# Performance work log

Hardware: AMD Instinct MI355X
Metric: run time of the kernel (lower is better)

The kernel has to match this reference:

```python
import jax, jax.numpy as jnp
import numpy as np

HIDDEN = 4096
N_HEADS = 32
N_KV_HEADS = 8
HEAD_DIM = 128
ROPE_THETA = 1e6
EPS = 1e-6
T = 2048


def setup_inputs() -> dict:
    key = jax.random.key(0)
    k1, k2, k3, k4, k5 = jax.random.split(key, 5)
    q_size = N_HEADS * HEAD_DIM
    kv_size = N_KV_HEADS * HEAD_DIM
    return {
        "positions": jnp.arange(T, dtype=jnp.int32),
        "hidden_states": jax.random.normal(k1, (T, HIDDEN), dtype=jnp.float32),
        "Wqkv": jax.random.normal(k2, (HIDDEN, q_size + 2 * kv_size), dtype=jnp.float32) * (HIDDEN ** -0.5),
        "Wo": jax.random.normal(k3, (q_size, HIDDEN), dtype=jnp.float32) * (q_size ** -0.5),
        "q_norm_w": jnp.ones((HEAD_DIM,), dtype=jnp.float32) + 0.01 * jax.random.normal(k4, (HEAD_DIM,), dtype=jnp.float32),
        "k_norm_w": jnp.ones((HEAD_DIM,), dtype=jnp.float32) + 0.01 * jax.random.normal(k5, (HEAD_DIM,), dtype=jnp.float32),
    }


def _rmsnorm(x, w):
    var = jnp.mean(jnp.square(x), axis=-1, keepdims=True)
    return x * jax.lax.rsqrt(var + EPS) * w


def _rope(x, positions):
    # NeoX-style rotate-half RoPE, rotary_dim == head_dim. x: [T, H, D]
    half = HEAD_DIM // 2
    inv_freq = 1.0 / (ROPE_THETA ** (jnp.arange(0, half, dtype=jnp.float32) / half))
    ang = positions.astype(jnp.float32)[:, None] * inv_freq  # [T, D/2]
    cos = jnp.cos(ang)[:, None, :]  # [T, 1, D/2]
    sin = jnp.sin(ang)[:, None, :]
    x1, x2 = x[..., :half], x[..., half:]
    return jnp.concatenate([x1 * cos - x2 * sin, x2 * cos + x1 * sin], axis=-1)


def reference(positions, hidden_states, Wqkv, Wo, q_norm_w, k_norm_w):
    q_size = N_HEADS * HEAD_DIM
    kv_size = N_KV_HEADS * HEAD_DIM
    qkv = hidden_states @ Wqkv  # [T, q+2kv]
    q = qkv[:, :q_size].reshape(-1, N_HEADS, HEAD_DIM)
    k = qkv[:, q_size:q_size + kv_size].reshape(-1, N_KV_HEADS, HEAD_DIM)
    v = qkv[:, q_size + kv_size:].reshape(-1, N_KV_HEADS, HEAD_DIM)
    q = _rmsnorm(q, q_norm_w)
    k = _rmsnorm(k, k_norm_w)
    q = _rope(q, positions)
    k = _rope(k, positions)
    rep = N_HEADS // N_KV_HEADS
    k = jnp.repeat(k, rep, axis=1)  # [T, 32, D]
    v = jnp.repeat(v, rep, axis=1)
    scale = HEAD_DIM ** -0.5
    scores = jnp.einsum('thd,shd->hts', q, k) * scale  # [H, T, T]
    t = hidden_states.shape[0]
    causal = jnp.tril(jnp.ones((t, t), dtype=bool))
    scores = jnp.where(causal[None, :, :], scores, jnp.finfo(scores.dtype).min)
    probs = jax.nn.softmax(scores, axis=-1)
    o = jnp.einsum('hts,shd->thd', probs, v)  # [T, H, D]
    return o.reshape(t, -1) @ Wo  # [T, hidden]
```

## Files before the change

kernel.cpp:

```cpp
#include <hip/hip_runtime.h>

#define T_SEQ 2048
#define HID   4096
#define NH    32
#define NKV   8
#define HD    128
#define QS    (NH*HD)
#define KVS   (NKV*HD)
#define QKVN  (QS + 2*KVS)

typedef unsigned short u16;
typedef __attribute__((ext_vector_type(8))) __bf16 bf16x8;
typedef __attribute__((ext_vector_type(8))) unsigned short u16x8;
typedef __attribute__((ext_vector_type(4))) unsigned short u16x4;
typedef __attribute__((ext_vector_type(4))) float f32x4;

__device__ __forceinline__ u16 f2bu(float x) {
  unsigned u = __builtin_bit_cast(unsigned, x);
  return (u16)((u + 0x7fffu + ((u >> 16) & 1u)) >> 16);
}
__device__ __forceinline__ float bu2f(u16 v) {
  unsigned u = ((unsigned)v) << 16;
  return __builtin_bit_cast(float, u);
}
__device__ __forceinline__ void gload16(const void* g, void* l) {
  __builtin_amdgcn_global_load_lds((const __attribute__((address_space(1))) void*)g,
                                   (__attribute__((address_space(3))) void*)l, 16, 0, 0);
}

__global__ void k_cvt(const float* __restrict__ in, u16* __restrict__ out, int n8) {
  for (int i = blockIdx.x * blockDim.x + threadIdx.x; i < n8; i += gridDim.x * blockDim.x) {
    const float4* p = (const float4*)in + (size_t)i * 2;
    float4 a = p[0], b = p[1];
    u16x8 v;
    v[0]=f2bu(a.x); v[1]=f2bu(a.y); v[2]=f2bu(a.z); v[3]=f2bu(a.w);
    v[4]=f2bu(b.x); v[5]=f2bu(b.y); v[6]=f2bu(b.z); v[7]=f2bu(b.w);
    *((u16x8*)out + i) = v;
  }
}

__global__ void k_transcvt(const float* __restrict__ in, u16* __restrict__ out, int R, int C) {
  __shared__ float tile[32][33];
  int c0 = blockIdx.x * 32, r0 = blockIdx.y * 32;
  int tx = threadIdx.x & 31, ty = threadIdx.x >> 5;
#pragma unroll
  for (int g = 0; g < 4; ++g)
    tile[ty + g * 8][tx] = in[(size_t)(r0 + ty + g * 8) * C + c0 + tx];
  __syncthreads();
#pragma unroll
  for (int g = 0; g < 4; ++g) {
    int cc = g * 8 + ty;
    out[(size_t)(c0 + cc) * R + r0 + tx] = f2bu(tile[tx][cc]);
  }
}

template<int OUTF32>
__global__ __launch_bounds__(256, 2)
void k_gemm(const u16* __restrict__ A, const u16* __restrict__ Bt,
            void* __restrict__ C, int K, int ldc) {
  __shared__ u16 sA[128 * 64];
  __shared__ u16 sB[128 * 64];
  const int tid = threadIdx.x;
  const int w = tid >> 6, lane = tid & 63, lo = lane & 15, hi = lane >> 4;
  const int wr = w >> 1, wc = w & 1;
  const int bm = blockIdx.y * 128, bn = blockIdx.x * 128;
  f32x4 acc[4][4] = {};
  const int nk = K >> 6;
  for (int kt = 0; kt < nk; ++kt) {
    const int kbase = kt * 64;
#pragma unroll
    for (int i = 0; i < 4; ++i) {
      int c = i * 256 + tid;
      int row = c >> 3, o8 = (c & 7) * 8;
      gload16(A + (size_t)(bm + row) * K + kbase + o8, sA + c * 8);
      gload16(Bt + (size_t)(bn + row) * K + kbase + o8, sB + c * 8);
    }
    __syncthreads();
#pragma unroll
    for (int kc = 0; kc < 2; ++kc) {
      bf16x8 af[4], bfr[4];
#pragma unroll
      for (int m = 0; m < 4; ++m)
        af[m] = *(const bf16x8*)(sA + (wr * 64 + m * 16 + lo) * 64 + kc * 32 + hi * 8);
#pragma unroll
      for (int n = 0; n < 4; ++n)
        bfr[n] = *(const bf16x8*)(sB + (wc * 64 + n * 16 + lo) * 64 + kc * 32 + hi * 8);
#pragma unroll
      for (int m = 0; m < 4; ++m)
#pragma unroll
        for (int n = 0; n < 4; ++n)
          acc[m][n] = __builtin_amdgcn_mfma_f32_16x16x32_bf16(af[m], bfr[n], acc[m][n], 0, 0, 0);
    }
    __syncthreads();
  }
#pragma unroll
  for (int m = 0; m < 4; ++m)
#pragma unroll
    for (int n = 0; n < 4; ++n) {
      int col = bn + wc * 64 + n * 16 + lo;
#pragma unroll
      for (int r = 0; r < 4; ++r) {
        int row = bm + wr * 64 + m * 16 + hi * 4 + r;
        float v = acc[m][n][r];
        if (OUTF32) ((float*)C)[(size_t)row * ldc + col] = v;
        else        ((u16*)C)[(size_t)row * ldc + col] = f2bu(v);
      }
    }
}

__global__ void k_normrope(const u16* __restrict__ qkv, const int* __restrict__ pos,
                           const float* __restrict__ qw, const float* __restrict__ kw,
                           u16* __restrict__ qb, u16* __restrict__ kb, u16* __restrict__ vb) {
  const int t = blockIdx.x;
  const int tid = threadIdx.x, w = tid >> 6, lane = tid & 63;
  const float p = (float)pos[t];
  const int d0 = lane * 2;
  const int j = d0 & 63;
  const float L2T_64 = 19.931568569324174f / 64.0f;
  float ang0 = p * exp2f(-(float)j * L2T_64);
  float ang1 = p * exp2f(-(float)(j + 1) * L2T_64);
  float c0 = cosf(ang0), s0 = sinf(ang0);
  float c1 = cosf(ang1), s1 = sinf(ang1);
  const bool hiHalf = lane >= 32;
  for (int it = 0; it < 10; ++it) {
    int h = it * 4 + w;
    bool isq = h < NH;
    int base = t * QKVN + (isq ? h * HD : QS + (h - NH) * HD);
    float x0 = bu2f(qkv[base + d0]);
    float x1 = bu2f(qkv[base + d0 + 1]);
    float ss = x0 * x0 + x1 * x1;
#pragma unroll
    for (int off = 1; off < 64; off <<= 1) ss += __shfl_xor(ss, off);
    float inv = rsqrtf(ss * (1.0f / 128.0f) + 1e-6f);
    const float* nw = isq ? qw : kw;
    float y0 = x0 * inv * nw[d0];
    float y1 = x1 * inv * nw[d0 + 1];
    float z0 = __shfl_xor(y0, 32);
    float z1 = __shfl_xor(y1, 32);
    float r0 = hiHalf ? (y0 * c0 + z0 * s0) : (y0 * c0 - z0 * s0);
    float r1 = hiHalf ? (y1 * c1 + z1 * s1) : (y1 * c1 - z1 * s1);
    u16* dst = isq ? (qb + ((size_t)h * T_SEQ + t) * HD)
                   : (kb + ((size_t)(h - NH) * T_SEQ + t) * HD);
    dst[d0] = f2bu(r0);
    dst[d0 + 1] = f2bu(r1);
  }
  for (int i = tid; i < KVS; i += 256) {
    int kvh = i >> 7, d = i & 127;
    vb[((size_t)kvh * T_SEQ + t) * HD + d] = qkv[t * QKVN + QS + KVS + i];
  }
}

__global__ __launch_bounds__(256, 4)
void k_attn(const u16* __restrict__ qb, const u16* __restrict__ kb,
            const u16* __restrict__ vb, u16* __restrict__ ao) {
  __shared__ u16 Ks[64 * 128];
  __shared__ u16 Vt[128 * 64];
  __shared__ u16 Ps[4][16 * 64];
  const int h = blockIdx.y, kvh = h >> 2;
  const int q0 = blockIdx.x * 64;
  const int tid = threadIdx.x, w = tid >> 6, lane = tid & 63, lo = lane & 15, hi = lane >> 4;
  const int lo7 = lane & 7;
  const int qr0 = q0 + w * 16;
  bf16x8 qf[4];
  const u16* Qp = qb + ((size_t)h * T_SEQ + qr0 + lo) * HD;
#pragma unroll
  for (int kc = 0; kc < 4; ++kc) qf[kc] = *(const bf16x8*)(Qp + kc * 32 + hi * 8);
  f32x4 o[8] = {};
  float mrow[4], ssum[4];
#pragma unroll
  for (int r = 0; r < 4; ++r) { mrow[r] = -1e30f; ssum[r] = 0.f; }
  const float scale = 0.08838834764831845f;
  const int nkt = blockIdx.x + 1;
  const u16* Kb = kb + (size_t)kvh * T_SEQ * HD;
  const u16* Vb = vb + (size_t)kvh * T_SEQ * HD;
  const int krow = tid >> 4;
  const int kg = (tid & 15) ^ (krow & 7);
  const int vkvc = tid & 15, vfc = tid >> 4;

  for (int kt = 0; kt < nkt; ++kt) {
#pragma unroll
    for (int i = 0; i < 4; ++i)
      gload16(Kb + (size_t)(kt * 64 + i * 16 + krow) * HD + kg * 8,
              Ks + i * 2048 + tid * 8);
    {
      u16x8 vv0 = *(const u16x8*)(Vb + (size_t)(kt * 64 + vkvc * 4 + 0) * HD + vfc * 8);
      u16x8 vv1 = *(const u16x8*)(Vb + (size_t)(kt * 64 + vkvc * 4 + 1) * HD + vfc * 8);
      u16x8 vv2 = *(const u16x8*)(Vb + (size_t)(kt * 64 + vkvc * 4 + 2) * HD + vfc * 8);
      u16x8 vv3 = *(const u16x8*)(Vb + (size_t)(kt * 64 + vkvc * 4 + 3) * HD + vfc * 8);
#pragma unroll
      for (int e = 0; e < 8; ++e) {
        int feat = vfc * 8 + e;
        int gp = (vkvc >> 1) ^ (feat & 7);
        u16x4 pk; pk[0] = vv0[e]; pk[1] = vv1[e]; pk[2] = vv2[e]; pk[3] = vv3[e];
        *(u16x4*)(Vt + feat * 64 + gp * 8 + (vkvc & 1) * 4) = pk;
      }
    }
    __syncthreads();
    f32x4 sa[4] = {};
#pragma unroll
    for (int kc = 0; kc < 4; ++kc) {
#pragma unroll
      for (int n = 0; n < 4; ++n) {
        int row = n * 16 + lo;
        bf16x8 kf = *(const bf16x8*)(Ks + row * 128 + (((kc * 4 + hi) ^ lo7) * 8));
        sa[n] = __builtin_amdgcn_mfma_f32_16x16x32_bf16(qf[kc], kf, sa[n], 0, 0, 0);
      }
    }
    float pvv[4][4], pmax[4];
#pragma unroll
    for (int r = 0; r < 4; ++r) {
      int qi = qr0 + hi * 4 + r;
      float pm = -1e30f;
#pragma unroll
      for (int n = 0; n < 4; ++n) {
        int kj = kt * 64 + n * 16 + lo;
        float sv = (kj <= qi) ? sa[n][r] * scale : -1e30f;
        pvv[n][r] = sv;
        pm = fmaxf(pm, sv);
      }
#pragma unroll
      for (int off = 1; off < 16; off <<= 1) pm = fmaxf(pm, __shfl_xor(pm, off));
      pmax[r] = pm;
    }
#pragma unroll
    for (int r = 0; r < 4; ++r) {
      float mnew = fmaxf(mrow[r], pmax[r]);
      float corr = __expf(mrow[r] - mnew);
      mrow[r] = mnew;
      float ps = 0.f;
#pragma unroll
      for (int n = 0; n < 4; ++n) {
        float p = __expf(pvv[n][r] - mnew);
        pvv[n][r] = p; ps += p;
      }
#pragma unroll
      for (int off = 1; off < 16; off <<= 1) ps += __shfl_xor(ps, off);
      ssum[r] = ssum[r] * corr + ps;
#pragma unroll
      for (int nf = 0; nf < 8; ++nf) o[nf][r] *= corr;
    }
    u16* Pw = Ps[w];
#pragma unroll
    for (int n = 0; n < 4; ++n) {
      int gcol = n * 2 + (lo >> 3);
#pragma unroll
      for (int r = 0; r < 4; ++r) {
        int row = hi * 4 + r;
        Pw[row * 64 + ((gcol ^ (row & 7)) * 8) + lo7] = f2bu(pvv[n][r]);
      }
    }
#pragma unroll
    for (int ks = 0; ks < 2; ++ks) {
      bf16x8 pf = *(const bf16x8*)(Pw + lo * 64 + (((ks * 4 + hi) ^ lo7) * 8));
#pragma unroll
      for (int nf = 0; nf < 8; ++nf) {
        int feat = nf * 16 + lo;
        bf16x8 vf = *(const bf16x8*)(Vt + feat * 64 + (((ks * 4 + hi) ^ lo7) * 8));
        o[nf] = __builtin_amdgcn_mfma_f32_16x16x32_bf16(pf, vf, o[nf], 0, 0, 0);
      }
    }
    __syncthreads();
  }
#pragma unroll
  for (int r = 0; r < 4; ++r) ssum[r] = 1.0f / ssum[r];
#pragma unroll
  for (int nf = 0; nf < 8; ++nf)
#pragma unroll
    for (int r = 0; r < 4; ++r) {
      int row = qr0 + hi * 4 + r;
      ao[(size_t)row * HID + h * HD + nf * 16 + lo] = f2bu(o[nf][r] * ssum[r]);
    }
}

extern "C" void kernel_launch(void* const* d_in, const int* in_sizes, int n_in,
                              void* d_out, int out_size, void* d_ws, size_t ws_size,
                              hipStream_t stream) {
  (void)in_sizes; (void)n_in; (void)out_size; (void)ws_size;
  const int*   positions = (const int*)d_in[0];
  const float* hs   = (const float*)d_in[1];
  const float* wqkv = (const float*)d_in[2];
  const float* wo   = (const float*)d_in[3];
  const float* qnw  = (const float*)d_in[4];
  const float* knw  = (const float*)d_in[5];
  char* ws = (char*)d_ws;

  u16* hsb   = (u16*)d_out;
  u16* qbuf  = (u16*)d_out + 8388608;
  u16* wqkvT = (u16*)(ws + 0);
  u16* woT   = (u16*)(ws + 50331648);
  u16* qkvb  = (u16*)(ws + 83886080);
  u16* kbuf  = (u16*)(ws + 109051904);
  u16* vbuf  = (u16*)(ws + 113246208);
  u16* aob   = (u16*)(ws + 0);

  k_cvt<<<2048, 256, 0, stream>>>(hs, hsb, (T_SEQ * HID) / 8);
  k_transcvt<<<dim3(QKVN / 32, HID / 32), 256, 0, stream>>>(wqkv, wqkvT, HID, QKVN);
  k_transcvt<<<dim3(HID / 32, QS / 32), 256, 0, stream>>>(wo, woT, QS, HID);
  k_gemm<0><<<dim3(QKVN / 128, T_SEQ / 128), 256, 0, stream>>>(hsb, wqkvT, qkvb, HID, QKVN);
  k_normrope<<<T_SEQ, 256, 0, stream>>>(qkvb, positions, qnw, knw, qbuf, kbuf, vbuf);
  k_attn<<<dim3(T_SEQ / 64, NH), 256, 0, stream>>>(qbuf, kbuf, vbuf, aob);
  k_gemm<1><<<dim3(HID / 128, T_SEQ / 128), 256, 0, stream>>>(aob, woT, d_out, QS, HID);
}
```

Before: 648.6 us.

## Pair causal attention query tiles per block and vectorize weight transpose-convert

Each attention block now handles two query tiles, x and 31-x, so every block does the same amount of causal work and the grid shrinks from 32x32 to 16x32 blocks. This removes the tail imbalance of the triangular causal workload. The weight transpose/convert kernel moves to 64x64 tiles with float4 loads and 16-byte bf16 stores to cut memory transactions. The risk is fewer blocks in flight for attention (512 on a large GPU) and more serial work per block.

```diff
diff --git a/kernel.cpp b/kernel.cpp
--- a/kernel.cpp
+++ b/kernel.cpp
@@ -40,18 +40,28 @@
 }
 
 __global__ void k_transcvt(const float* __restrict__ in, u16* __restrict__ out, int R, int C) {
-  __shared__ float tile[32][33];
-  int c0 = blockIdx.x * 32, r0 = blockIdx.y * 32;
-  int tx = threadIdx.x & 31, ty = threadIdx.x >> 5;
-#pragma unroll
-  for (int g = 0; g < 4; ++g)
-    tile[ty + g * 8][tx] = in[(size_t)(r0 + ty + g * 8) * C + c0 + tx];
+  __shared__ float tile[64][65];
+  const int c0 = blockIdx.x * 64, r0 = blockIdx.y * 64;
+  const int tid = threadIdx.x;
+  const int row = tid >> 2, c4 = (tid & 3) * 4;
+#pragma unroll
+  for (int j = 0; j < 4; ++j) {
+    float4 a = *(const float4*)(in + (size_t)(r0 + row) * C + c0 + c4 + j * 16);
+    tile[row][c4 + j * 16 + 0] = a.x;
+    tile[row][c4 + j * 16 + 1] = a.y;
+    tile[row][c4 + j * 16 + 2] = a.z;
+    tile[row][c4 + j * 16 + 3] = a.w;
+  }
   __syncthreads();
-#pragma unroll
-  for (int g = 0; g < 4; ++g) {
-    int cc = g * 8 + ty;
-    out[(size_t)(c0 + cc) * R + r0 + tx] = f2bu(tile[tx][cc]);
-  }
+  const int col = tid >> 2, rq = (tid & 3) * 16;
+  u16x8 v0, v1;
+#pragma unroll
+  for (int j = 0; j < 8; ++j) v0[j] = f2bu(tile[rq + j][col]);
+#pragma unroll
+  for (int j = 0; j < 8; ++j) v1[j] = f2bu(tile[rq + 8 + j][col]);
+  u16* dst = out + (size_t)(c0 + col) * R + r0 + rq;
+  *(u16x8*)(dst) = v0;
+  *(u16x8*)(dst + 8) = v1;
 }
 
 template<int OUTF32>
@@ -157,119 +167,123 @@
   __shared__ u16 Vt[128 * 64];
   __shared__ u16 Ps[4][16 * 64];
   const int h = blockIdx.y, kvh = h >> 2;
-  const int q0 = blockIdx.x * 64;
   const int tid = threadIdx.x, w = tid >> 6, lane = tid & 63, lo = lane & 15, hi = lane >> 4;
   const int lo7 = lane & 7;
-  const int qr0 = q0 + w * 16;
-  bf16x8 qf[4];
-  const u16* Qp = qb + ((size_t)h * T_SEQ + qr0 + lo) * HD;
-#pragma unroll
-  for (int kc = 0; kc < 4; ++kc) qf[kc] = *(const bf16x8*)(Qp + kc * 32 + hi * 8);
-  f32x4 o[8] = {};
-  float mrow[4], ssum[4];
-#pragma unroll
-  for (int r = 0; r < 4; ++r) { mrow[r] = -1e30f; ssum[r] = 0.f; }
   const float scale = 0.08838834764831845f;
-  const int nkt = blockIdx.x + 1;
   const u16* Kb = kb + (size_t)kvh * T_SEQ * HD;
   const u16* Vb = vb + (size_t)kvh * T_SEQ * HD;
   const int krow = tid >> 4;
   const int kg = (tid & 15) ^ (krow & 7);
   const int vkvc = tid & 15, vfc = tid >> 4;
 
-  for (int kt = 0; kt < nkt; ++kt) {
-#pragma unroll
-    for (int i = 0; i < 4; ++i)
-      gload16(Kb + (size_t)(kt * 64 + i * 16 + krow) * HD + kg * 8,
-              Ks + i * 2048 + tid * 8);
-    {
-      u16x8 vv0 = *(const u16x8*)(Vb + (size_t)(kt * 64 + vkvc * 4 + 0) * HD + vfc * 8);
-      u16x8 vv1 = *(const u16x8*)(Vb + (size_t)(kt * 64 + vkvc * 4 + 1) * HD + vfc * 8);
-      u16x8 vv2 = *(const u16x8*)(Vb + (size_t)(kt * 64 + vkvc * 4 + 2) * HD + vfc * 8);
-      u16x8 vv3 = *(const u16x8*)(Vb + (size_t)(kt * 64 + vkvc * 4 + 3) * HD + vfc * 8);
-#pragma unroll
-      for (int e = 0; e < 8; ++e) {
-        int feat = vfc * 8 + e;
-        int gp = (vkvc >> 1) ^ (feat & 7);
-        u16x4 pk; pk[0] = vv0[e]; pk[1] = vv1[e]; pk[2] = vv2[e]; pk[3] = vv3[e];
-        *(u16x4*)(Vt + feat * 64 + gp * 8 + (vkvc & 1) * 4) = pk;
-      }
+  for (int item = 0; item < 2; ++item) {
+    const int xb = item == 0 ? blockIdx.x : 31 - blockIdx.x;
+    const int q0 = xb * 64;
+    const int nkt = xb + 1;
+    const int qr0 = q0 + w * 16;
+    bf16x8 qf[4];
+    const u16* Qp = qb + ((size_t)h * T_SEQ + qr0 + lo) * HD;
+#pragma unroll
+    for (int kc = 0; kc < 4; ++kc) qf[kc] = *(const bf16x8*)(Qp + kc * 32 + hi * 8);
+    f32x4 o[8] = {};
+    float mrow[4], ssum[4];
+#pragma unroll
+    for (int r = 0; r < 4; ++r) { mrow[r] = -1e30f; ssum[r] = 0.f; }
+
+    for (int kt = 0; kt < nkt; ++kt) {
+#pragma unroll
+      for (int i = 0; i < 4; ++i)
+        gload16(Kb + (size_t)(kt * 64 + i * 16 + krow) * HD + kg * 8,
+                Ks + i * 2048 + tid * 8);
+      {
+        u16x8 vv0 = *(const u16x8*)(Vb + (size_t)(kt * 64 + vkvc * 4 + 0) * HD + vfc * 8);
+        u16x8 vv1 = *(const u16x8*)(Vb + (size_t)(kt * 64 + vkvc * 4 + 1) * HD + vfc * 8);
+        u16x8 vv2 = *(const u16x8*)(Vb + (size_t)(kt * 64 + vkvc * 4 + 2) * HD + vfc * 8);
+        u16x8 vv3 = *(const u16x8*)(Vb + (size_t)(kt * 64 + vkvc * 4 + 3) * HD + vfc * 8);
+#pragma unroll
+        for (int e = 0; e < 8; ++e) {
+          int feat = vfc * 8 + e;
+          int gp = (vkvc >> 1) ^ (feat & 7);
+          u16x4 pk; pk[0] = vv0[e]; pk[1] = vv1[e]; pk[2] = vv2[e]; pk[3] = vv3[e];
+          *(u16x4*)(Vt + feat * 64 + gp * 8 + (vkvc & 1) * 4) = pk;
+        }
+      }
+      __syncthreads();
+      f32x4 sa[4] = {};
+#pragma unroll
+      for (int kc = 0; kc < 4; ++kc) {
+#pragma unroll
+        for (int n = 0; n < 4; ++n) {
+          int row = n * 16 + lo;
+          bf16x8 kf = *(const bf16x8*)(Ks + row * 128 + (((kc * 4 + hi) ^ lo7) * 8));
+          sa[n] = __builtin_amdgcn_mfma_f32_16x16x32_bf16(qf[kc], kf, sa[n], 0, 0, 0);
+        }
+      }
+      float pvv[4][4], pmax[4];
+#pragma unroll
+      for (int r = 0; r < 4; ++r) {
+        int qi = qr0 + hi * 4 + r;
+        float pm = -1e30f;
+#pragma unroll
+        for (int n = 0; n < 4; ++n) {
+          int kj = kt * 64 + n * 16 + lo;
+          float sv = (kj <= qi) ? sa[n][r] * scale : -1e30f;
+          pvv[n][r] = sv;
+          pm = fmaxf(pm, sv);
+        }
+#pragma unroll
+        for (int off = 1; off < 16; off <<= 1) pm = fmaxf(pm, __shfl_xor(pm, off));
+        pmax[r] = pm;
+      }
+#pragma unroll
+      for (int r = 0; r < 4; ++r) {
+        float mnew = fmaxf(mrow[r], pmax[r]);
+        float corr = __expf(mrow[r] - mnew);
+        mrow[r] = mnew;
+        float ps = 0.f;
+#pragma unroll
+        for (int n = 0; n < 4; ++n) {
+          float p = __expf(pvv[n][r] - mnew);
+          pvv[n][r] = p; ps += p;
+        }
+#pragma unroll
+        for (int off = 1; off < 16; off <<= 1) ps += __shfl_xor(ps, off);
+        ssum[r] = ssum[r] * corr + ps;
+#pragma unroll
+        for (int nf = 0; nf < 8; ++nf) o[nf][r] *= corr;
+      }
+      u16* Pw = Ps[w];
+#pragma unroll
+      for (int n = 0; n < 4; ++n) {
+        int gcol = n * 2 + (lo >> 3);
+#pragma unroll
+        for (int r = 0; r < 4; ++r) {
+          int row = hi * 4 + r;
+          Pw[row * 64 + ((gcol ^ (row & 7)) * 8) + lo7] = f2bu(pvv[n][r]);
+        }
+      }
+#pragma unroll
+      for (int ks = 0; ks < 2; ++ks) {
+        bf16x8 pf = *(const bf16x8*)(Pw + lo * 64 + (((ks * 4 + hi) ^ lo7) * 8));
+#pragma unroll
+        for (int nf = 0; nf < 8; ++nf) {
+          int feat = nf * 16 + lo;
+          bf16x8 vf = *(const bf16x8*)(Vt + feat * 64 + (((ks * 4 + hi) ^ lo7) * 8));
+          o[nf] = __builtin_amdgcn_mfma_f32_16x16x32_bf16(pf, vf, o[nf], 0, 0, 0);
+        }
+      }
+      __syncthreads();
     }
-    __syncthreads();
-    f32x4 sa[4] = {};
-#pragma unroll
-    for (int kc = 0; kc < 4; ++kc) {
-#pragma unroll
-      for (int n = 0; n < 4; ++n) {
-        int row = n * 16 + lo;
-        bf16x8 kf = *(const bf16x8*)(Ks + row * 128 + (((kc * 4 + hi) ^ lo7) * 8));
-        sa[n] = __builtin_amdgcn_mfma_f32_16x16x32_bf16(qf[kc], kf, sa[n], 0, 0, 0);
-      }
-    }
-    float pvv[4][4], pmax[4];
-#pragma unroll
-    for (int r = 0; r < 4; ++r) {
-      int qi = qr0 + hi * 4 + r;
-      float pm = -1e30f;
-#pragma unroll
-      for (int n = 0; n < 4; ++n) {
-        int kj = kt * 64 + n * 16 + lo;
-        float sv = (kj <= qi) ? sa[n][r] * scale : -1e30f;
-        pvv[n][r] = sv;
-        pm = fmaxf(pm, sv);
-      }
-#pragma unroll
-      for (int off = 1; off < 16; off <<= 1) pm = fmaxf(pm, __shfl_xor(pm, off));
-      pmax[r] = pm;
-    }
-#pragma unroll
-    for (int r = 0; r < 4; ++r) {
-      float mnew = fmaxf(mrow[r], pmax[r]);
-      float corr = __expf(mrow[r] - mnew);
-      mrow[r] = mnew;
-      float ps = 0.f;
-#pragma unroll
-      for (int n = 0; n < 4; ++n) {
-        float p = __expf(pvv[n][r] - mnew);
-        pvv[n][r] = p; ps += p;
-      }
-#pragma unroll
-      for (int off = 1; off < 16; off <<= 1) ps += __shfl_xor(ps, off);
-      ssum[r] = ssum[r] * corr + ps;
-#pragma unroll
-      for (int nf = 0; nf < 8; ++nf) o[nf][r] *= corr;
-    }
-    u16* Pw = Ps[w];
-#pragma unroll
-    for (int n = 0; n < 4; ++n) {
-      int gcol = n * 2 + (lo >> 3);
+#pragma unroll
+    for (int r = 0; r < 4; ++r) ssum[r] = 1.0f / ssum[r];
+#pragma unroll
+    for (int nf = 0; nf < 8; ++nf)
 #pragma unroll
       for (int r = 0; r < 4; ++r) {
-        int row = hi * 4 + r;
-        Pw[row * 64 + ((gcol ^ (row & 7)) * 8) + lo7] = f2bu(pvv[n][r]);
-      }
-    }
-#pragma unroll
-    for (int ks = 0; ks < 2; ++ks) {
-      bf16x8 pf = *(const bf16x8*)(Pw + lo * 64 + (((ks * 4 + hi) ^ lo7) * 8));
-#pragma unroll
-      for (int nf = 0; nf < 8; ++nf) {
-        int feat = nf * 16 + lo;
-        bf16x8 vf = *(const bf16x8*)(Vt + feat * 64 + (((ks * 4 + hi) ^ lo7) * 8));
-        o[nf] = __builtin_amdgcn_mfma_f32_16x16x32_bf16(pf, vf, o[nf], 0, 0, 0);
-      }
-    }
-    __syncthreads();
-  }
-#pragma unroll
-  for (int r = 0; r < 4; ++r) ssum[r] = 1.0f / ssum[r];
-#pragma unroll
-  for (int nf = 0; nf < 8; ++nf)
-#pragma unroll
-    for (int r = 0; r < 4; ++r) {
-      int row = qr0 + hi * 4 + r;
-      ao[(size_t)row * HID + h * HD + nf * 16 + lo] = f2bu(o[nf][r] * ssum[r]);
-    }
+        int row = qr0 + hi * 4 + r;
+        ao[(size_t)row * HID + h * HD + nf * 16 + lo] = f2bu(o[nf][r] * ssum[r]);
+      }
+  }
 }
 
 extern "C" void kernel_launch(void* const* d_in, const int* in_sizes, int n_in,
@@ -294,10 +308,10 @@
   u16* aob   = (u16*)(ws + 0);
 
   k_cvt<<<2048, 256, 0, stream>>>(hs, hsb, (T_SEQ * HID) / 8);
-  k_transcvt<<<dim3(QKVN / 32, HID / 32), 256, 0, stream>>>(wqkv, wqkvT, HID, QKVN);
-  k_transcvt<<<dim3(HID / 32, QS / 32), 256, 0, stream>>>(wo, woT, QS, HID);
+  k_transcvt<<<dim3(QKVN / 64, HID / 64), 256, 0, stream>>>(wqkv, wqkvT, HID, QKVN);
+  k_transcvt<<<dim3(HID / 64, QS / 64), 256, 0, stream>>>(wo, woT, QS, HID);
   k_gemm<0><<<dim3(QKVN / 128, T_SEQ / 128), 256, 0, stream>>>(hsb, wqkvT, qkvb, HID, QKVN);
   k_normrope<<<T_SEQ, 256, 0, stream>>>(qkvb, positions, qnw, knw, qbuf, kbuf, vbuf);
-  k_attn<<<dim3(T_SEQ / 64, NH), 256, 0, stream>>>(qbuf, kbuf, vbuf, aob);
+  k_attn<<<dim3(16, NH), 256, 0, stream>>>(qbuf, kbuf, vbuf, aob);
   k_gemm<1><<<dim3(HID / 128, T_SEQ / 128), 256, 0, stream>>>(aob, woT, d_out, QS, HID);
 }
```

After: 593.4 us. 8.5% less time.
